# Kernel tuning notes

Hardware: AMD Instinct MI355X
Metric: run time of the kernel (lower is better)

The kernel has to match this reference:

```python
import jax, jax.numpy as jnp
import numpy as np

E = 8            # num_experts
DIM = 2880       # model dim
HID = 2880       # expert hidden dim (mlp1 outputs 2*HID, interleaved glu/linear)
T = 16384        # total dispatched tokens, evenly split across experts
SWIGLU_LIMIT = 7.0
ALPHA = 1.702


def swiglu(x, alpha=ALPHA, limit=SWIGLU_LIMIT):
    # interleaved: even channels -> glu gate, odd channels -> linear
    x_glu = x[..., ::2]
    x_lin = x[..., 1::2]
    x_glu = jnp.minimum(x_glu, limit)
    x_lin = jnp.clip(x_lin, -limit, limit)
    return x_glu * jax.nn.sigmoid(alpha * x_glu) * (x_lin + 1.0)


def setup_inputs() -> dict:
    key = jax.random.key(0)
    k1, k2, k3, k4, k5 = jax.random.split(key, 5)
    scale = 0.02
    x = jax.random.normal(k1, (T, DIM), dtype=jnp.float32)
    num_tokens_per_expert = jnp.full((E,), T // E, dtype=jnp.int64)
    mlp1_weight = jax.random.normal(k2, (E, 2 * HID, DIM), dtype=jnp.float32) * scale
    mlp1_bias = jax.random.normal(k3, (E, 2 * HID), dtype=jnp.float32) * scale
    mlp2_weight = jax.random.normal(k4, (E, DIM, HID), dtype=jnp.float32) * scale
    mlp2_bias = jax.random.normal(k5, (E, DIM), dtype=jnp.float32) * scale
    return {
        "x": x,
        "num_tokens_per_expert": num_tokens_per_expert,
        "mlp1_weight": mlp1_weight,
        "mlp1_bias": mlp1_bias,
        "mlp2_weight": mlp2_weight,
        "mlp2_bias": mlp2_bias,
    }


def reference(x, num_tokens_per_expert, mlp1_weight, mlp1_bias, mlp2_weight, mlp2_bias):
    # Equal token counts per expert (as constructed): grouped GEMM == batched GEMM
    # over a reshaped [E, T/E, DIM] view. tp_degree == 1 so ScaleBiasForward is identity.
    tpe = T // E
    xg = x.reshape(E, tpe, DIM)                                  # [E, t, D]
    h = jnp.einsum("etd,ehd->eth", xg, mlp1_weight)              # [E, t, 2H]
    h = h + mlp1_bias[:, None, :]
    h = swiglu(h)                                                # [E, t, H]
    out = jnp.einsum("eth,edh->etd", h, mlp2_weight)             # [E, t, D]
    out = out + mlp2_bias[:, None, :]
    return out.reshape(T, DIM)
```

## Files before the change

### kernel.cpp

```cpp
#include <hip/hip_runtime.h>
#include <hip/hip_bf16.h>


#define TT   16384
#define DIM_ 2880
#define HID_ 2880
#define NE   8
#define TPE  2048
#define KDIM 2880
#define NT   45

typedef __attribute__((ext_vector_type(8))) short short8;
typedef __attribute__((ext_vector_type(4))) float f32x4;

__device__ __forceinline__ unsigned short f2bf(float f) {
  unsigned u = __builtin_bit_cast(unsigned, f);
  u += 0x7fffu + ((u >> 16) & 1u);
  return (unsigned short)(u >> 16);
}

__global__ void __launch_bounds__(256) cvt_f32_bf16(const float* __restrict__ src,
                                                    unsigned short* __restrict__ dst,
                                                    long n) {
  long i = ((long)blockIdx.x * 256 + threadIdx.x) * 8;
  if (i >= n) return;
  float4 a = *(const float4*)(src + i);
  float4 b = *(const float4*)(src + i + 4);
  union { unsigned short u[8]; short8 v; } r;
  r.u[0] = f2bf(a.x); r.u[1] = f2bf(a.y); r.u[2] = f2bf(a.z); r.u[3] = f2bf(a.w);
  r.u[4] = f2bf(b.x); r.u[5] = f2bf(b.y); r.u[6] = f2bf(b.z); r.u[7] = f2bf(b.w);
  *(short8*)(dst + i) = r.v;
}

template<bool FUSE_SWIGLU>
__global__ void __launch_bounds__(512, 2) gemm8(const unsigned short* __restrict__ A,
                                                const unsigned short* __restrict__ B,
                                                const float* __restrict__ bias,
                                                void* __restrict__ Cout,
                                                int M, int N) {
  __shared__ unsigned short As[2][256 * 64];
  __shared__ unsigned short Bs[2][192 * 64];

  const int tid  = threadIdx.x;
  const int lane = tid & 63;
  const int wid  = tid >> 6;
  const int wr   = wid >> 2;
  const int wc   = wid & 3;
  const int e    = blockIdx.z;

  const int ntn   = N / 192;
  const int ntm   = M / 256;
  const int per_e = ntn * ntm;
  const int bid   = blockIdx.x;
  const int swz   = (bid & 7) * (per_e >> 3) + (bid >> 3);
  const int m0    = (swz / ntn) * 256;
  const int n0    = (swz % ntn) * 192;

  const int srow = tid >> 3;
  const int scol = (((tid & 7) ^ (srow & 7)) << 4) >> 1;
  const unsigned short* Aexp = A + ((size_t)e * M + m0 + srow) * KDIM + scol;
  const unsigned short* Bexp = B + ((size_t)e * N + n0 + srow) * KDIM + scol;

  auto stage = [&](int buf, int kt) {
    const unsigned short* asrc = Aexp + (size_t)kt * 64;
#pragma unroll
    for (int j = 0; j < 4; ++j)
      __builtin_amdgcn_global_load_lds(
          (const __attribute__((address_space(1))) unsigned int*)(asrc + (size_t)(j * 64) * KDIM),
          (__attribute__((address_space(3))) unsigned int*)(&As[buf][j * 4096 + tid * 8]),
          16, 0, 0);
    const unsigned short* bsrc = Bexp + (size_t)kt * 64;
#pragma unroll
    for (int j = 0; j < 3; ++j)
      __builtin_amdgcn_global_load_lds(
          (const __attribute__((address_space(1))) unsigned int*)(bsrc + (size_t)(j * 64) * KDIM),
          (__attribute__((address_space(3))) unsigned int*)(&Bs[buf][j * 4096 + tid * 8]),
          16, 0, 0);
  };

  const int arow_off = (wr * 128 + (lane & 15)) * 128;
  const int brow_off = (wc * 48  + (lane & 15)) * 128;
  const int swzb = (lane & 7) << 4;
  const int kb   = ((lane >> 4) & 3) * 16;
  const int c0 = kb ^ swzb;
  const int c1 = (64 + kb) ^ swzb;

  f32x4 acc[8][3] = {};

  stage(0, 0);
  stage(1, 1);
  asm volatile("s_waitcnt vmcnt(7)" ::: "memory");
  __builtin_amdgcn_s_barrier();

  for (int t = 0; t < NT; ++t) {
    const int cur = t & 1;
    const char* aB = (const char*)(&As[cur][0]) + arow_off;
    const char* bB = (const char*)(&Bs[cur][0]) + brow_off;

    short8 a0[8], a1[8], b0[3], b1[3];
#pragma unroll
    for (int fm = 0; fm < 8; ++fm) {
      a0[fm] = *(const short8*)(aB + fm * 2048 + c0);
      a1[fm] = *(const short8*)(aB + fm * 2048 + c1);
    }
#pragma unroll
    for (int fn = 0; fn < 3; ++fn) {
      b0[fn] = *(const short8*)(bB + fn * 2048 + c0);
      b1[fn] = *(const short8*)(bB + fn * 2048 + c1);
    }

#pragma unroll
    for (int fn = 0; fn < 3; ++fn)
#pragma unroll
      for (int fm = 0; fm < 8; ++fm)
        acc[fm][fn] = __builtin_amdgcn_mfma_f32_16x16x32_bf16(a0[fm], b0[fn], acc[fm][fn], 0, 0, 0);

    asm volatile("s_waitcnt lgkmcnt(0)" ::: "memory");
    __builtin_amdgcn_s_barrier();

    const bool more = (t + 2 < NT);
    if (more) stage(cur, t + 2);

    __builtin_amdgcn_s_setprio(1);
#pragma unroll
    for (int fn = 0; fn < 3; ++fn)
#pragma unroll
      for (int fm = 0; fm < 8; ++fm)
        acc[fm][fn] = __builtin_amdgcn_mfma_f32_16x16x32_bf16(a1[fm], b1[fn], acc[fm][fn], 0, 0, 0);
    __builtin_amdgcn_s_setprio(0);

    if (more) asm volatile("s_waitcnt vmcnt(7)" ::: "memory");
    else      asm volatile("s_waitcnt vmcnt(0)" ::: "memory");
    __builtin_amdgcn_s_barrier();
  }

  const float* be = bias + (size_t)e * N;
  if constexpr (FUSE_SWIGLU) {
    unsigned short* ha = (unsigned short*)Cout + (size_t)e * M * (N >> 1);
#pragma unroll
    for (int fm = 0; fm < 8; ++fm)
#pragma unroll
      for (int fn = 0; fn < 3; ++fn) {
        const int col = n0 + wc * 48 + fn * 16 + (lane & 15);
        const float bc = be[col];
#pragma unroll
        for (int j = 0; j < 4; ++j) {
          const int row = m0 + wr * 128 + fm * 16 + (lane >> 4) * 4 + j;
          float v = acc[fm][fn][j] + bc;
          float p = __shfl_xor(v, 1);
          if (!(lane & 1)) {
            float g  = fminf(v, 7.0f);
            float l2 = fminf(fmaxf(p, -7.0f), 7.0f);
            float act = g / (1.0f + __expf(-1.702f * g)) * (l2 + 1.0f);
            ha[(size_t)row * (N >> 1) + (col >> 1)] = f2bf(act);
          }
        }
      }
  } else {
    float* out = (float*)Cout + (size_t)e * M * N;
#pragma unroll
    for (int fm = 0; fm < 8; ++fm)
#pragma unroll
      for (int fn = 0; fn < 3; ++fn) {
        const int col = n0 + wc * 48 + fn * 16 + (lane & 15);
        const float bc = be[col];
#pragma unroll
        for (int j = 0; j < 4; ++j) {
          const int row = m0 + wr * 128 + fm * 16 + (lane >> 4) * 4 + j;
          out[(size_t)row * N + col] = acc[fm][fn][j] + bc;
        }
      }
  }
}

extern "C" void kernel_launch(void* const* d_in, const int* in_sizes, int n_in,
                              void* d_out, int out_size, void* d_ws, size_t ws_size,
                              hipStream_t stream) {
  const float* x  = (const float*)d_in[0];
  const float* w1 = (const float*)d_in[2];
  const float* b1 = (const float*)d_in[3];
  const float* w2 = (const float*)d_in[4];
  const float* b2 = (const float*)d_in[5];

  unsigned short* xb  = (unsigned short*)d_ws;
  unsigned short* w1b = xb  + (size_t)TT * DIM_;
  unsigned short* w2b = w1b + (size_t)NE * 2 * HID_ * DIM_;
  unsigned short* ha  = w2b + (size_t)NE * DIM_ * HID_;

  const long nx = (long)TT * DIM_;
  const long n1 = (long)NE * 2 * HID_ * DIM_;
  const long n2 = (long)NE * DIM_ * HID_;
  cvt_f32_bf16<<<(int)(nx / 2048), 256, 0, stream>>>(x,  xb,  nx);
  cvt_f32_bf16<<<(int)(n1 / 2048), 256, 0, stream>>>(w1, w1b, n1);
  cvt_f32_bf16<<<(int)(n2 / 2048), 256, 0, stream>>>(w2, w2b, n2);

  dim3 g1((5760 / 192) * (TPE / 256), 1, NE);
  gemm8<true><<<g1, 512, 0, stream>>>(xb, w1b, b1, ha, TPE, 5760);

  dim3 g2((DIM_ / 192) * (TPE / 256), 1, NE);
  gemm8<false><<<g2, 512, 0, stream>>>(ha, w2b, b2, (float*)d_out, TPE, DIM_);
}
```

Before: 1.252 ms.

## Widen GEMM N-tile to 320 and split K-step into four ping-pong MFMA phases

Enlarges the block's N tile from 192 to 320 (5 fragments per wave) so each A tile is reused across more output columns, raising arithmetic intensity per LDS and global load. The inner K-step is restructured into four smaller phases that interleave LDS fragment reads with MFMA bursts, separated by barriers and priority changes, to overlap LDS traffic with matrix math. The cost is more accumulator registers (8x5 f32x4), more LDS for B, fewer blocks per expert, and extra barriers per iteration.

```diff
diff --git a/kernel.cpp b/kernel.cpp
--- a/kernel.cpp
+++ b/kernel.cpp
@@ -33,13 +33,13 @@
 }
 
 template<bool FUSE_SWIGLU>
-__global__ void __launch_bounds__(512, 2) gemm8(const unsigned short* __restrict__ A,
-                                                const unsigned short* __restrict__ B,
-                                                const float* __restrict__ bias,
-                                                void* __restrict__ Cout,
-                                                int M, int N) {
+__global__ void __launch_bounds__(512, 2) gemm4p(const unsigned short* __restrict__ A,
+                                                 const unsigned short* __restrict__ B,
+                                                 const float* __restrict__ bias,
+                                                 void* __restrict__ Cout,
+                                                 int M, int N) {
   __shared__ unsigned short As[2][256 * 64];
-  __shared__ unsigned short Bs[2][192 * 64];
+  __shared__ unsigned short Bs[2][320 * 64];
 
   const int tid  = threadIdx.x;
   const int lane = tid & 63;
@@ -48,16 +48,16 @@
   const int wc   = wid & 3;
   const int e    = blockIdx.z;
 
-  const int ntn   = N / 192;
+  const int ntn   = N / 320;
   const int ntm   = M / 256;
   const int per_e = ntn * ntm;
   const int bid   = blockIdx.x;
   const int swz   = (bid & 7) * (per_e >> 3) + (bid >> 3);
   const int m0    = (swz / ntn) * 256;
-  const int n0    = (swz % ntn) * 192;
+  const int n0    = (swz % ntn) * 320;
 
   const int srow = tid >> 3;
-  const int scol = (((tid & 7) ^ (srow & 7)) << 4) >> 1;
+  const int scol = ((tid & 7) ^ (srow & 7)) << 3;
   const unsigned short* Aexp = A + ((size_t)e * M + m0 + srow) * KDIM + scol;
   const unsigned short* Bexp = B + ((size_t)e * N + n0 + srow) * KDIM + scol;
 
@@ -71,65 +71,89 @@
           16, 0, 0);
     const unsigned short* bsrc = Bexp + (size_t)kt * 64;
 #pragma unroll
-    for (int j = 0; j < 3; ++j)
+    for (int j = 0; j < 5; ++j)
       __builtin_amdgcn_global_load_lds(
           (const __attribute__((address_space(1))) unsigned int*)(bsrc + (size_t)(j * 64) * KDIM),
           (__attribute__((address_space(3))) unsigned int*)(&Bs[buf][j * 4096 + tid * 8]),
           16, 0, 0);
   };
 
-  const int arow_off = (wr * 128 + (lane & 15)) * 128;
-  const int brow_off = (wc * 48  + (lane & 15)) * 128;
+  const int arow = (wr * 128 + (lane & 15)) * 128;
+  const int brow = (wc * 80  + (lane & 15)) * 128;
   const int swzb = (lane & 7) << 4;
   const int kb   = ((lane >> 4) & 3) * 16;
   const int c0 = kb ^ swzb;
   const int c1 = (64 + kb) ^ swzb;
 
-  f32x4 acc[8][3] = {};
+  f32x4 acc[8][5] = {};
 
   stage(0, 0);
   stage(1, 1);
-  asm volatile("s_waitcnt vmcnt(7)" ::: "memory");
+  asm volatile("s_waitcnt vmcnt(9)" ::: "memory");
   __builtin_amdgcn_s_barrier();
 
   for (int t = 0; t < NT; ++t) {
     const int cur = t & 1;
-    const char* aB = (const char*)(&As[cur][0]) + arow_off;
-    const char* bB = (const char*)(&Bs[cur][0]) + brow_off;
-
-    short8 a0[8], a1[8], b0[3], b1[3];
-#pragma unroll
-    for (int fm = 0; fm < 8; ++fm) {
-      a0[fm] = *(const short8*)(aB + fm * 2048 + c0);
-      a1[fm] = *(const short8*)(aB + fm * 2048 + c1);
-    }
-#pragma unroll
-    for (int fn = 0; fn < 3; ++fn) {
-      b0[fn] = *(const short8*)(bB + fn * 2048 + c0);
-      b1[fn] = *(const short8*)(bB + fn * 2048 + c1);
-    }
-
-#pragma unroll
-    for (int fn = 0; fn < 3; ++fn)
-#pragma unroll
-      for (int fm = 0; fm < 8; ++fm)
-        acc[fm][fn] = __builtin_amdgcn_mfma_f32_16x16x32_bf16(a0[fm], b0[fn], acc[fm][fn], 0, 0, 0);
-
+    const char* aB = (const char*)(&As[cur][0]) + arow;
+    const char* bB = (const char*)(&Bs[cur][0]) + brow;
+
+    short8 a[4], a2[4], b0[5], b1[5];
+
+#pragma unroll
+    for (int i = 0; i < 4; ++i) a[i] = *(const short8*)(aB + i * 2048 + c0);
+#pragma unroll
+    for (int f = 0; f < 5; ++f) b0[f] = *(const short8*)(bB + f * 2048 + c0);
+    __builtin_amdgcn_s_barrier();
     asm volatile("s_waitcnt lgkmcnt(0)" ::: "memory");
+    __builtin_amdgcn_s_setprio(1);
+#pragma unroll
+    for (int f = 0; f < 5; ++f)
+#pragma unroll
+      for (int i = 0; i < 4; ++i)
+        acc[i][f] = __builtin_amdgcn_mfma_f32_16x16x32_bf16(a[i], b0[f], acc[i][f], 0, 0, 0);
+    __builtin_amdgcn_s_setprio(0);
+    __builtin_amdgcn_s_barrier();
+
+#pragma unroll
+    for (int i = 0; i < 4; ++i) a[i] = *(const short8*)(aB + (4 + i) * 2048 + c0);
+    __builtin_amdgcn_s_barrier();
+    asm volatile("s_waitcnt lgkmcnt(0)" ::: "memory");
+    __builtin_amdgcn_s_setprio(1);
+#pragma unroll
+    for (int f = 0; f < 5; ++f)
+#pragma unroll
+      for (int i = 0; i < 4; ++i)
+        acc[4 + i][f] = __builtin_amdgcn_mfma_f32_16x16x32_bf16(a[i], b0[f], acc[4 + i][f], 0, 0, 0);
+    __builtin_amdgcn_s_setprio(0);
+    __builtin_amdgcn_s_barrier();
+
+#pragma unroll
+    for (int i = 0; i < 4; ++i) a[i]  = *(const short8*)(aB + i * 2048 + c1);
+#pragma unroll
+    for (int f = 0; f < 5; ++f) b1[f] = *(const short8*)(bB + f * 2048 + c1);
+#pragma unroll
+    for (int i = 0; i < 4; ++i) a2[i] = *(const short8*)(aB + (4 + i) * 2048 + c1);
+    __builtin_amdgcn_s_barrier();
+    asm volatile("s_waitcnt lgkmcnt(0)" ::: "memory");
+    __builtin_amdgcn_s_setprio(1);
+#pragma unroll
+    for (int f = 0; f < 5; ++f)
+#pragma unroll
+      for (int i = 0; i < 4; ++i)
+        acc[i][f] = __builtin_amdgcn_mfma_f32_16x16x32_bf16(a[i], b1[f], acc[i][f], 0, 0, 0);
+    __builtin_amdgcn_s_setprio(0);
     __builtin_amdgcn_s_barrier();
 
     const bool more = (t + 2 < NT);
     if (more) stage(cur, t + 2);
-
-    __builtin_amdgcn_s_setprio(1);
-#pragma unroll
-    for (int fn = 0; fn < 3; ++fn)
-#pragma unroll
-      for (int fm = 0; fm < 8; ++fm)
-        acc[fm][fn] = __builtin_amdgcn_mfma_f32_16x16x32_bf16(a1[fm], b1[fn], acc[fm][fn], 0, 0, 0);
-    __builtin_amdgcn_s_setprio(0);
-
-    if (more) asm volatile("s_waitcnt vmcnt(7)" ::: "memory");
+    __builtin_amdgcn_s_setprio(1);
+#pragma unroll
+    for (int f = 0; f < 5; ++f)
+#pragma unroll
+      for (int i = 0; i < 4; ++i)
+        acc[4 + i][f] = __builtin_amdgcn_mfma_f32_16x16x32_bf16(a2[i], b1[f], acc[4 + i][f], 0, 0, 0);
+    __builtin_amdgcn_s_setprio(0);
+    if (more) asm volatile("s_waitcnt vmcnt(9)" ::: "memory");
     else      asm volatile("s_waitcnt vmcnt(0)" ::: "memory");
     __builtin_amdgcn_s_barrier();
   }
@@ -140,8 +164,8 @@
 #pragma unroll
     for (int fm = 0; fm < 8; ++fm)
 #pragma unroll
-      for (int fn = 0; fn < 3; ++fn) {
-        const int col = n0 + wc * 48 + fn * 16 + (lane & 15);
+      for (int fn = 0; fn < 5; ++fn) {
+        const int col = n0 + wc * 80 + fn * 16 + (lane & 15);
         const float bc = be[col];
 #pragma unroll
         for (int j = 0; j < 4; ++j) {
@@ -161,8 +185,8 @@
 #pragma unroll
     for (int fm = 0; fm < 8; ++fm)
 #pragma unroll
-      for (int fn = 0; fn < 3; ++fn) {
-        const int col = n0 + wc * 48 + fn * 16 + (lane & 15);
+      for (int fn = 0; fn < 5; ++fn) {
+        const int col = n0 + wc * 80 + fn * 16 + (lane & 15);
         const float bc = be[col];
 #pragma unroll
         for (int j = 0; j < 4; ++j) {
@@ -194,9 +218,9 @@
   cvt_f32_bf16<<<(int)(n1 / 2048), 256, 0, stream>>>(w1, w1b, n1);
   cvt_f32_bf16<<<(int)(n2 / 2048), 256, 0, stream>>>(w2, w2b, n2);
 
-  dim3 g1((5760 / 192) * (TPE / 256), 1, NE);
-  gemm8<true><<<g1, 512, 0, stream>>>(xb, w1b, b1, ha, TPE, 5760);
-
-  dim3 g2((DIM_ / 192) * (TPE / 256), 1, NE);
-  gemm8<false><<<g2, 512, 0, stream>>>(ha, w2b, b2, (float*)d_out, TPE, DIM_);
-}
+  dim3 g1((5760 / 320) * (TPE / 256), 1, NE);
+  gemm4p<true><<<g1, 512, 0, stream>>>(xb, w1b, b1, ha, TPE, 5760);
+
+  dim3 g2((DIM_ / 320) * (TPE / 256), 1, NE);
+  gemm4p<false><<<g2, 512, 0, stream>>>(ha, w2b, b2, (float*)d_out, TPE, DIM_);
+}
```

New measurement: 1.381 ms. 10.3% more time.
